# Optimization experiments

Measured on AMD Instinct MI355X. Metric: run time of the kernel, lower is better.

Reference implementation:

```python
import jax, jax.numpy as jnp
import numpy as np

B, S, D, K = 4, 4096, 1024, 64

def setup_inputs() -> dict:
    key = jax.random.key(0)
    kx, kq, kk, kv, ko = jax.random.split(key, 5)
    scale = 1.0 / np.sqrt(D)
    return {
        "x": jax.random.normal(kx, (B, S, D), dtype=jnp.float32),
        "Wq": jax.random.uniform(kq, (K, D), dtype=jnp.float32, minval=-scale, maxval=scale),
        "Wk": jax.random.uniform(kk, (K, D), dtype=jnp.float32, minval=-scale, maxval=scale),
        "Wv": jax.random.uniform(kv, (K, D), dtype=jnp.float32, minval=-scale, maxval=scale),
        "Wo": jax.random.uniform(ko, (D, K), dtype=jnp.float32, minval=-1.0/np.sqrt(K), maxval=1.0/np.sqrt(K)),
    }

def reference(x, Wq, Wk, Wv, Wo):
    # projections: torch Linear(dim, key_dim, bias=False) -> x @ W.T
    Q = jax.nn.elu(x @ Wq.T) + 1.0          # [B,S,K]
    Kf = jax.nn.elu(x @ Wk.T) + 1.0         # [B,S,K]
    V = x @ Wv.T                             # [B,S,K]
    # causal running KV state via cumsum of outer products: [B,S,K,K]
    KV_sum = jnp.cumsum(Kf[..., :, None] * V[..., None, :], axis=1)
    K_sum = jnp.cumsum(Kf, axis=1)           # [B,S,K]
    num = jnp.einsum('bsk,bskm->bsm', Q, KV_sum)   # [B,S,K]
    den = jnp.einsum('bsk,bsk->bs', Q, K_sum)[..., None]
    out = num / (den + 1e-6)
    return out @ Wo.T                         # [B,S,D]
```

## Files before the change

### kernel.cpp

```cpp
#include <hip/hip_runtime.h>

#define BB 4
#define SS 4096
#define DDIM 1024
#define KDIM 64
#define NCHUNK 64
#define TCHUNK 256
#define MROWS 16384

typedef short short8v __attribute__((ext_vector_type(8)));
typedef float f32x4 __attribute__((ext_vector_type(4)));
#define MFMA16 __builtin_amdgcn_mfma_f32_16x16x32_bf16

__device__ __forceinline__ ushort f2bf(float f) {
    uint u = __float_as_uint(f);
    u += 0x7FFFu + ((u >> 16) & 1u);
    return (ushort)(u >> 16);
}

__global__ __launch_bounds__(256) void k_wconv(
    const float* __restrict__ Wq, const float* __restrict__ Wk,
    const float* __restrict__ Wv, const float* __restrict__ Wo,
    ushort* __restrict__ Whf, ushort* __restrict__ Wof)
{
    const int b = blockIdx.x, t = threadIdx.x;
    const int ks = t >> 7;
    const int l = (t >> 1) & 63;
    const int half = t & 1;
    if (b < 192) {
        const int s = b / 12, cf = b % 12;
        const int grow = cf * 16 + (l & 15);
        const int gcol = s * 64 + ks * 32 + ((l >> 4) & 3) * 8 + half * 4;
        const float* src = (grow < 64) ? (Wq + (size_t)grow * DDIM)
                         : (grow < 128) ? (Wk + (size_t)(grow - 64) * DDIM)
                                        : (Wv + (size_t)(grow - 128) * DDIM);
        float4 v = *(const float4*)&src[gcol];
        ushort* dst = &Whf[(size_t)(((s * 12 + cf) * 2 + ks) * 64 + l) * 8 + half * 4];
        dst[0] = f2bf(v.x); dst[1] = f2bf(v.y); dst[2] = f2bf(v.z); dst[3] = f2bf(v.w);
    } else {
        const int cf = b - 192;
        const int d = cf * 16 + (l & 15);
        const int kc = ks * 32 + ((l >> 4) & 3) * 8 + half * 4;
        float4 v = *(const float4*)&Wo[(size_t)d * KDIM + kc];
        ushort* dst = &Wof[(size_t)((cf * 2 + ks) * 64 + l) * 8 + half * 4];
        dst[0] = f2bf(v.x); dst[1] = f2bf(v.y); dst[2] = f2bf(v.z); dst[3] = f2bf(v.w);
    }
}

#define EBP 216
__global__ __launch_bounds__(256) void k_proj(
    const float* __restrict__ x, const ushort* __restrict__ Whf,
    ushort* __restrict__ Qf, ushort* __restrict__ Kff,
    ushort* __restrict__ KfT, ushort* __restrict__ VT)
{
    __shared__ ushort xs[32 * 512];
    const int t = threadIdx.x;
    const int w = t >> 6, l = t & 63;
    const int mb = blockIdx.x;
    const int row0 = mb * 32;

    f32x4 acc[2][3];
#pragma unroll
    for (int r = 0; r < 2; ++r)
#pragma unroll
        for (int c = 0; c < 3; ++c) acc[r][c] = (f32x4){0.f, 0.f, 0.f, 0.f};

    auto stageX = [&](int h) {
#pragma unroll
        for (int i = 0; i < 8; ++i) {
            const int fidx = i * 256 + t;
            const int r = fidx >> 6;
            const int c = (fidx & 63) * 8;
            const float* p = &x[(size_t)(row0 + r) * DDIM + h * 512 + c];
            float4 u0 = *(const float4*)p;
            float4 u1 = *(const float4*)(p + 4);
            short8v hh;
            hh[0] = (short)f2bf(u0.x); hh[1] = (short)f2bf(u0.y);
            hh[2] = (short)f2bf(u0.z); hh[3] = (short)f2bf(u0.w);
            hh[4] = (short)f2bf(u1.x); hh[5] = (short)f2bf(u1.y);
            hh[6] = (short)f2bf(u1.z); hh[7] = (short)f2bf(u1.w);
            const int frag = (r >> 4) * 16 + (c >> 5);
            const int slot = ((r & 15) | (((c >> 3) & 3) << 4)) ^ (frag & 7);
            *(short8v*)&xs[(size_t)(frag * 64 + slot) * 8] = hh;
        }
    };
    auto loadW = [&](int sg, short8v (&bw)[6]) {
#pragma unroll
        for (int j = 0; j < 6; ++j) {
            const int cf = w * 3 + (j >> 1);
            const int f = cf * 2 + (j & 1);
            bw[j] = *(const short8v*)&Whf[((size_t)(sg * 24 + f)) * 512 + l * 8];
        }
    };
    auto computeStep = [&](int sl, short8v (&bw)[6]) {
#pragma unroll
        for (int ks = 0; ks < 2; ++ks) {
            const int kkl = sl * 2 + ks;
            const int f0 = kkl, f1 = 16 + kkl;
            short8v a0 = *(const short8v*)&xs[(size_t)(f0 * 64 + (l ^ (f0 & 7))) * 8];
            short8v a1 = *(const short8v*)&xs[(size_t)(f1 * 64 + (l ^ (f1 & 7))) * 8];
#pragma unroll
            for (int c = 0; c < 3; ++c) {
                acc[0][c] = MFMA16(a0, bw[c * 2 + ks], acc[0][c], 0, 0, 0);
                acc[1][c] = MFMA16(a1, bw[c * 2 + ks], acc[1][c], 0, 0, 0);
            }
        }
    };

    for (int h = 0; h < 2; ++h) {
        if (h) __syncthreads();
        stageX(h);
        __syncthreads();
        short8v bwA[6], bwB[6];
        loadW(h * 8, bwA);
        for (int s = 0; s < 8; s += 2) {
            loadW(h * 8 + s + 1, bwB);
            computeStep(s, bwA);
            if (s + 2 < 8) loadW(h * 8 + s + 2, bwA);
            computeStep(s + 1, bwB);
        }
    }

    __syncthreads();
    ushort* eb = xs;
#pragma unroll
    for (int rf = 0; rf < 2; ++rf)
#pragma unroll
        for (int c = 0; c < 3; ++c) {
            const int col = w * 48 + c * 16 + (l & 15);
#pragma unroll
            for (int q = 0; q < 4; ++q) {
                const int rl = rf * 16 + ((l >> 4) << 2) + q;
                float v = acc[rf][c][q];
                if (col < 128) v = (v > 0.f) ? v + 1.f : __expf(v);
                eb[rl * EBP + col] = f2bf(v);
            }
        }
    __syncthreads();

    {
        const int rf = t >> 7, ks = (t >> 6) & 1, lam = t & 63;
        const int r = rf * 16 + (lam & 15);
        const int c0 = ks * 32 + ((lam >> 4) & 3) * 8;
        short8v q8 = *(const short8v*)&eb[r * EBP + c0];
        short8v k8 = *(const short8v*)&eb[r * EBP + 64 + c0];
        const size_t fo = ((size_t)(mb * 4 + rf * 2 + ks)) * 512 + lam * 8;
        *(short8v*)&Qf[fo] = q8;
        *(short8v*)&Kff[fo] = k8;
    }
    {
        const int f = t >> 6, lam = t & 63;
        const int kcol = 64 + f * 16 + (lam & 15);
        const int vcol = 128 + f * 16 + (lam & 15);
        const int jb = ((lam >> 4) & 3) * 8;
        short8v kT, vT;
#pragma unroll
        for (int e = 0; e < 8; ++e) {
            kT[e] = (short)eb[(jb + e) * EBP + kcol];
            vT[e] = (short)eb[(jb + e) * EBP + vcol];
        }
        const size_t fo = ((size_t)((mb >> 1) * 8 + f * 2 + (mb & 1))) * 512 + lam * 8;
        *(short8v*)&KfT[fo] = kT;
        *(short8v*)&VT[fo] = vT;
    }
}

__global__ __launch_bounds__(64) void k_chunksum(
    const ushort* __restrict__ KfT, const ushort* __restrict__ VT,
    float* __restrict__ KVc, float* __restrict__ Ksc)
{
    const int g = blockIdx.x, l = threadIdx.x;
    short8v ka[4][2], vb[4][2];
#pragma unroll
    for (int f = 0; f < 4; ++f)
#pragma unroll
        for (int js = 0; js < 2; ++js) {
            const size_t fo = ((size_t)(g * 8 + f * 2 + js)) * 512 + l * 8;
            ka[f][js] = *(const short8v*)&KfT[fo];
            vb[f][js] = *(const short8v*)&VT[fo];
        }
    short8v onesf;
#pragma unroll
    for (int e = 0; e < 8; ++e) onesf[e] = ((l & 15) == 0) ? (short)0x3F80 : (short)0;

    f32x4 acc[4][5];
#pragma unroll
    for (int kf = 0; kf < 4; ++kf)
#pragma unroll
        for (int mf = 0; mf < 5; ++mf) acc[kf][mf] = (f32x4){0.f, 0.f, 0.f, 0.f};
#pragma unroll
    for (int js = 0; js < 2; ++js)
#pragma unroll
        for (int kf = 0; kf < 4; ++kf) {
#pragma unroll
            for (int mf = 0; mf < 4; ++mf)
                acc[kf][mf] = MFMA16(ka[kf][js], vb[mf][js], acc[kf][mf], 0, 0, 0);
            acc[kf][4] = MFMA16(ka[kf][js], onesf, acc[kf][4], 0, 0, 0);
        }
    const int lq = l >> 4;
#pragma unroll
    for (int kf = 0; kf < 4; ++kf) {
#pragma unroll
        for (int q = 0; q < 4; ++q) {
            const int k = kf * 16 + lq * 4 + q;
#pragma unroll
            for (int mf = 0; mf < 4; ++mf)
                KVc[(size_t)g * 4096 + k * 64 + mf * 16 + (l & 15)] = acc[kf][mf][q];
            if ((l & 15) == 0) Ksc[(size_t)g * KDIM + k] = acc[kf][4][q];
        }
    }
}

__global__ void k_scan(const float* __restrict__ KVc, const float* __restrict__ Ksc,
                       float* __restrict__ Sst, float* __restrict__ Kss)
{
    const int b = blockIdx.x / 65;
    const int r = blockIdx.x % 65;
    const int t = threadIdx.x;
    if (r < 64) {
        const int e = r * 64 + t;
        float v[64];
#pragma unroll
        for (int i = 0; i < 64; ++i)
            v[i] = KVc[((size_t)(b * NCHUNK + i)) * 4096 + e];
        float acc = 0.f;
#pragma unroll
        for (int i = 0; i < 64; ++i) {
            Sst[((size_t)(b * NCHUNK + i)) * 4096 + e] = acc;
            acc += v[i];
        }
    } else {
        float v[64];
#pragma unroll
        for (int i = 0; i < 64; ++i)
            v[i] = Ksc[((size_t)(b * NCHUNK + i)) * KDIM + t];
        float acc = 0.f;
#pragma unroll
        for (int i = 0; i < 64; ++i) {
            Kss[((size_t)(b * NCHUNK + i)) * KDIM + t] = acc;
            acc += v[i];
        }
    }
}

__global__ __launch_bounds__(256) void k_intra(
    const ushort* __restrict__ Qf, const ushort* __restrict__ Kff,
    const ushort* __restrict__ VT, const float* __restrict__ Sst,
    const float* __restrict__ Kss, const ushort* __restrict__ Wof,
    float* __restrict__ out)
{
    __shared__ ushort pb[64 * 64];
    __shared__ ushort sT[80 * 64];
    __shared__ float ob[4][16 * 68 + 4];
    const int g = blockIdx.x, t = threadIdx.x;
    const int w = t >> 6, l = t & 63;
    const int lq = l >> 4;

    {
        const int k = t >> 2, m0 = (t & 3) * 16;
        const float4* sp = (const float4*)&Sst[(size_t)g * 4096 + k * 64 + m0];
        float4 f0 = sp[0], f1 = sp[1], f2v = sp[2], f3 = sp[3];
        float fv[16] = {f0.x, f0.y, f0.z, f0.w, f1.x, f1.y, f1.z, f1.w,
                        f2v.x, f2v.y, f2v.z, f2v.w, f3.x, f3.y, f3.z, f3.w};
#pragma unroll
        for (int i = 0; i < 16; ++i) {
            const int m = m0 + i;
            sT[m * 64 + (k ^ ((m & 7) << 3))] = f2bf(fv[i]);
        }
        if (t < 64) sT[64 * 64 + t] = f2bf(Kss[(size_t)g * KDIM + t]);
        for (int idx = t; idx < 960; idx += 256) sT[65 * 64 + idx] = 0;
    }

    short8v qa[2], kb[4][2];
    {
        const int mb = g * 2 + (w >> 1), rf = w & 1;
#pragma unroll
        for (int ks = 0; ks < 2; ++ks)
            qa[ks] = *(const short8v*)&Qf[((size_t)(mb * 4 + rf * 2 + ks)) * 512 + l * 8];
#pragma unroll
        for (int cf = 0; cf < 4; ++cf)
#pragma unroll
            for (int ks = 0; ks < 2; ++ks)
                kb[cf][ks] = *(const short8v*)&Kff[((size_t)((g * 2 + (cf >> 1)) * 4 + (cf & 1) * 2 + ks)) * 512 + l * 8];
    }
    f32x4 accs[4];
#pragma unroll
    for (int cf = 0; cf < 4; ++cf) accs[cf] = (f32x4){0.f, 0.f, 0.f, 0.f};
#pragma unroll
    for (int ks = 0; ks < 2; ++ks)
#pragma unroll
        for (int cf = 0; cf < 4; ++cf)
            accs[cf] = MFMA16(qa[ks], kb[cf][ks], accs[cf], 0, 0, 0);
#pragma unroll
    for (int cf = 0; cf < 4; ++cf)
#pragma unroll
        for (int q = 0; q < 4; ++q) {
            const int row = w * 16 + lq * 4 + q;
            const int col = cf * 16 + (l & 15);
            const float sv = (col <= row) ? accs[cf][q] : 0.f;
            pb[row * 64 + (col ^ ((row & 7) << 3))] = f2bf(sv);
        }
    __syncthreads();

    f32x4 accn[5];
#pragma unroll
    for (int mf = 0; mf < 5; ++mf) accn[mf] = (f32x4){0.f, 0.f, 0.f, 0.f};
    short8v onesf;
#pragma unroll
    for (int e = 0; e < 8; ++e) onesf[e] = ((l & 15) == 0) ? (short)0x3F80 : (short)0;
#pragma unroll
    for (int js = 0; js < 2; ++js) {
        const int prow = w * 16 + (l & 15);
        const int pbase = js * 32 + ((l >> 4) & 3) * 8;
        short8v pa = *(const short8v*)&pb[prow * 64 + (pbase ^ ((prow & 7) << 3))];
#pragma unroll
        for (int mf = 0; mf < 4; ++mf) {
            short8v vb = *(const short8v*)&VT[((size_t)(g * 8 + mf * 2 + js)) * 512 + l * 8];
            accn[mf] = MFMA16(pa, vb, accn[mf], 0, 0, 0);
        }
        accn[4] = MFMA16(pa, onesf, accn[4], 0, 0, 0);
    }
#pragma unroll
    for (int ks = 0; ks < 2; ++ks) {
        const int base = ks * 32 + ((l >> 4) & 3) * 8;
#pragma unroll
        for (int mf = 0; mf < 5; ++mf) {
            const int row = mf * 16 + (l & 15);
            short8v sb = *(const short8v*)&sT[row * 64 + (base ^ ((row & 7) << 3))];
            accn[mf] = MFMA16(qa[ks], sb, accn[mf], 0, 0, 0);
        }
    }
#pragma unroll
    for (int q = 0; q < 4; ++q) {
        const float den = __shfl(accn[4][q], (l & 48));
        const float rinv = 1.f / (den + 1e-6f);
        const int row = w * 16 + lq * 4 + q;
#pragma unroll
        for (int mf = 0; mf < 4; ++mf) {
            const int col = mf * 16 + (l & 15);
            pb[row * 64 + (col ^ ((row & 7) << 3))] = f2bf(accn[mf][q] * rinv);
        }
    }
    __syncthreads();

    short8v oa[4][2];
#pragma unroll
    for (int rf = 0; rf < 4; ++rf)
#pragma unroll
        for (int ks = 0; ks < 2; ++ks) {
            const int row = rf * 16 + (l & 15);
            const int base = ks * 32 + ((l >> 4) & 3) * 8;
            oa[rf][ks] = *(const short8v*)&pb[row * 64 + (base ^ ((row & 7) << 3))];
        }
    float* obw = ob[w];
#pragma unroll
    for (int rr = 0; rr < 4; ++rr) {
        f32x4 acco[4][4];
#pragma unroll
        for (int rf = 0; rf < 4; ++rf)
#pragma unroll
            for (int ci = 0; ci < 4; ++ci) acco[rf][ci] = (f32x4){0.f, 0.f, 0.f, 0.f};
#pragma unroll
        for (int ci = 0; ci < 4; ++ci) {
            const int cfg = w * 16 + rr * 4 + ci;
#pragma unroll
            for (int ks = 0; ks < 2; ++ks) {
                short8v wb = *(const short8v*)&Wof[((size_t)(cfg * 2 + ks)) * 512 + l * 8];
#pragma unroll
                for (int rf = 0; rf < 4; ++rf)
                    acco[rf][ci] = MFMA16(oa[rf][ks], wb, acco[rf][ci], 0, 0, 0);
            }
        }
#pragma unroll
        for (int rf = 0; rf < 4; ++rf) {
#pragma unroll
            for (int ci = 0; ci < 4; ++ci)
#pragma unroll
                for (int q = 0; q < 4; ++q)
                    obw[(lq * 4 + q) * 68 + ci * 16 + (l & 15)] = acco[rf][ci][q];
#pragma unroll
            for (int rg = 0; rg < 4; ++rg) {
                const int row = rg * 4 + lq;
                float4 vv = *(const float4*)&obw[row * 68 + (l & 15) * 4];
                *(float4*)&out[((size_t)(g * 64 + rf * 16 + row)) * DDIM
                               + w * 256 + rr * 64 + (l & 15) * 4] = vv;
            }
        }
    }
}

extern "C" void kernel_launch(void* const* d_in, const int* in_sizes, int n_in,
                              void* d_out, int out_size, void* d_ws, size_t ws_size,
                              hipStream_t stream)
{
    const float* x  = (const float*)d_in[0];
    const float* Wq = (const float*)d_in[1];
    const float* Wk = (const float*)d_in[2];
    const float* Wv = (const float*)d_in[3];
    const float* Wo = (const float*)d_in[4];
    float* out = (float*)d_out;

    float* ws   = (float*)d_ws;
    float* KVc  = ws;
    float* Sst  = KVc + (size_t)TCHUNK * 4096;
    float* Ksc  = Sst + (size_t)TCHUNK * 4096;
    float* Kss  = Ksc + (size_t)TCHUNK * KDIM;
    ushort* Whf = (ushort*)(Kss + (size_t)TCHUNK * KDIM);
    ushort* Wof = Whf + (size_t)192 * DDIM;
    ushort* Qf  = Wof + (size_t)64 * 1024;
    ushort* Kff = Qf  + (size_t)512 * 4 * 512;
    ushort* KfT = Kff + (size_t)512 * 4 * 512;
    ushort* VT  = KfT + (size_t)256 * 8 * 512;

    k_wconv<<<dim3(256), dim3(256), 0, stream>>>(Wq, Wk, Wv, Wo, Whf, Wof);
    k_proj<<<dim3(MROWS / 32), dim3(256), 0, stream>>>(x, Whf, Qf, Kff, KfT, VT);
    k_chunksum<<<dim3(TCHUNK), dim3(64), 0, stream>>>(KfT, VT, KVc, Ksc);
    k_scan<<<dim3(BB * 65), dim3(64), 0, stream>>>(KVc, Ksc, Sst, Kss);
    k_intra<<<dim3(TCHUNK), dim3(256), 0, stream>>>(Qf, Kff, VT, Sst, Kss, Wof, out);
}
```

Before: 58.01 us.

## Fuse chunk-sum into projection kernel and split intra kernel into half-chunks

The projection kernel now runs one 512-thread block per 64-row chunk. It computes the per-chunk K^T V and K sums directly from shared memory, which removes the k_chunksum launch and the KfT global round-trip. The x staging is double-buffered, so the second half's global loads are issued into registers before the first half's MFMA loop runs. The intra kernel is split into two blocks per chunk, each handling 32 rows, which doubles grid parallelism for the output projection. The trade-offs are more shared memory and registers per block in k_proj, fewer k_proj blocks, and redundant per-block loads of S state and Wo in k_intra.

```diff
diff --git a/kernel.cpp b/kernel.cpp
--- a/kernel.cpp
+++ b/kernel.cpp
@@ -48,32 +48,39 @@
 }
 
 #define EBP 216
-__global__ __launch_bounds__(256) void k_proj(
+__global__ __launch_bounds__(512) void k_proj(
     const float* __restrict__ x, const ushort* __restrict__ Whf,
-    ushort* __restrict__ Qf, ushort* __restrict__ Kff,
-    ushort* __restrict__ KfT, ushort* __restrict__ VT)
+    ushort* __restrict__ Qf, ushort* __restrict__ Kff, ushort* __restrict__ VT,
+    float* __restrict__ KVc, float* __restrict__ Ksc)
 {
-    __shared__ ushort xs[32 * 512];
+    __shared__ ushort xs[2 * 64 * 512];
     const int t = threadIdx.x;
     const int w = t >> 6, l = t & 63;
-    const int mb = blockIdx.x;
-    const int row0 = mb * 32;
-
-    f32x4 acc[2][3];
-#pragma unroll
-    for (int r = 0; r < 2; ++r)
-#pragma unroll
-        for (int c = 0; c < 3; ++c) acc[r][c] = (f32x4){0.f, 0.f, 0.f, 0.f};
-
-    auto stageX = [&](int h) {
+    const int rw = w >> 2, cw = w & 3;
+    const int g = blockIdx.x;
+    const int row0 = g * 64;
+    const int lq = l >> 4;
+
+    float4 xr[16];
+    auto stageLoad = [&](int h) {
 #pragma unroll
         for (int i = 0; i < 8; ++i) {
-            const int fidx = i * 256 + t;
+            const int fidx = i * 512 + t;
             const int r = fidx >> 6;
             const int c = (fidx & 63) * 8;
             const float* p = &x[(size_t)(row0 + r) * DDIM + h * 512 + c];
-            float4 u0 = *(const float4*)p;
-            float4 u1 = *(const float4*)(p + 4);
+            xr[i * 2] = *(const float4*)p;
+            xr[i * 2 + 1] = *(const float4*)(p + 4);
+        }
+    };
+    auto stageWrite = [&](int buf) {
+        ushort* xb = xs + buf * 32768;
+#pragma unroll
+        for (int i = 0; i < 8; ++i) {
+            const int fidx = i * 512 + t;
+            const int r = fidx >> 6;
+            const int c = (fidx & 63) * 8;
+            float4 u0 = xr[i * 2], u1 = xr[i * 2 + 1];
             short8v hh;
             hh[0] = (short)f2bf(u0.x); hh[1] = (short)f2bf(u0.y);
             hh[2] = (short)f2bf(u0.z); hh[3] = (short)f2bf(u0.w);
@@ -81,24 +88,33 @@
             hh[6] = (short)f2bf(u1.z); hh[7] = (short)f2bf(u1.w);
             const int frag = (r >> 4) * 16 + (c >> 5);
             const int slot = ((r & 15) | (((c >> 3) & 3) << 4)) ^ (frag & 7);
-            *(short8v*)&xs[(size_t)(frag * 64 + slot) * 8] = hh;
+            *(short8v*)&xb[(size_t)(frag * 64 + slot) * 8] = hh;
         }
     };
+
+    f32x4 acc[2][3];
+#pragma unroll
+    for (int r = 0; r < 2; ++r)
+#pragma unroll
+        for (int c = 0; c < 3; ++c) acc[r][c] = (f32x4){0.f, 0.f, 0.f, 0.f};
+
     auto loadW = [&](int sg, short8v (&bw)[6]) {
 #pragma unroll
         for (int j = 0; j < 6; ++j) {
-            const int cf = w * 3 + (j >> 1);
+            const int cf = cw * 3 + (j >> 1);
             const int f = cf * 2 + (j & 1);
             bw[j] = *(const short8v*)&Whf[((size_t)(sg * 24 + f)) * 512 + l * 8];
         }
     };
-    auto computeStep = [&](int sl, short8v (&bw)[6]) {
+    auto computeStep = [&](int buf, int sl, short8v (&bw)[6]) {
+        const ushort* xb = xs + buf * 32768;
 #pragma unroll
         for (int ks = 0; ks < 2; ++ks) {
             const int kkl = sl * 2 + ks;
-            const int f0 = kkl, f1 = 16 + kkl;
-            short8v a0 = *(const short8v*)&xs[(size_t)(f0 * 64 + (l ^ (f0 & 7))) * 8];
-            short8v a1 = *(const short8v*)&xs[(size_t)(f1 * 64 + (l ^ (f1 & 7))) * 8];
+            const int f0 = (rw * 2) * 16 + kkl;
+            const int f1 = (rw * 2 + 1) * 16 + kkl;
+            short8v a0 = *(const short8v*)&xb[(size_t)(f0 * 64 + (l ^ (f0 & 7))) * 8];
+            short8v a1 = *(const short8v*)&xb[(size_t)(f1 * 64 + (l ^ (f1 & 7))) * 8];
 #pragma unroll
             for (int c = 0; c < 3; ++c) {
                 acc[0][c] = MFMA16(a0, bw[c * 2 + ks], acc[0][c], 0, 0, 0);
@@ -107,31 +123,42 @@
         }
     };
 
-    for (int h = 0; h < 2; ++h) {
-        if (h) __syncthreads();
-        stageX(h);
-        __syncthreads();
+    stageLoad(0); stageWrite(0);
+    __syncthreads();
+    stageLoad(1);
+    {
         short8v bwA[6], bwB[6];
-        loadW(h * 8, bwA);
+        loadW(0, bwA);
         for (int s = 0; s < 8; s += 2) {
-            loadW(h * 8 + s + 1, bwB);
-            computeStep(s, bwA);
-            if (s + 2 < 8) loadW(h * 8 + s + 2, bwA);
-            computeStep(s + 1, bwB);
-        }
-    }
-
+            loadW(s + 1, bwB);
+            computeStep(0, s, bwA);
+            if (s + 2 < 8) loadW(s + 2, bwA);
+            computeStep(0, s + 1, bwB);
+        }
+    }
+    stageWrite(1);
     __syncthreads();
+    {
+        short8v bwA[6], bwB[6];
+        loadW(8, bwA);
+        for (int s = 0; s < 8; s += 2) {
+            loadW(8 + s + 1, bwB);
+            computeStep(1, s, bwA);
+            if (s + 2 < 8) loadW(8 + s + 2, bwA);
+            computeStep(1, s + 1, bwB);
+        }
+    }
+
     ushort* eb = xs;
 #pragma unroll
-    for (int rf = 0; rf < 2; ++rf)
-#pragma unroll
-        for (int c = 0; c < 3; ++c) {
-            const int col = w * 48 + c * 16 + (l & 15);
+    for (int rfi = 0; rfi < 2; ++rfi)
+#pragma unroll
+        for (int ci = 0; ci < 3; ++ci) {
+            const int col = (cw * 3 + ci) * 16 + (l & 15);
 #pragma unroll
             for (int q = 0; q < 4; ++q) {
-                const int rl = rf * 16 + ((l >> 4) << 2) + q;
-                float v = acc[rf][c][q];
+                const int rl = (rw * 2 + rfi) * 16 + lq * 4 + q;
+                float v = acc[rfi][ci][q];
                 if (col < 128) v = (v > 0.f) ? v + 1.f : __expf(v);
                 eb[rl * EBP + col] = f2bf(v);
             }
@@ -139,74 +166,57 @@
     __syncthreads();
 
     {
-        const int rf = t >> 7, ks = (t >> 6) & 1, lam = t & 63;
-        const int r = rf * 16 + (lam & 15);
+        const int fj = t >> 6, lam = t & 63;
+        const int rh = fj >> 2, rfm = (fj >> 1) & 1, ks = fj & 1;
+        const int r = rh * 32 + rfm * 16 + (lam & 15);
         const int c0 = ks * 32 + ((lam >> 4) & 3) * 8;
         short8v q8 = *(const short8v*)&eb[r * EBP + c0];
         short8v k8 = *(const short8v*)&eb[r * EBP + 64 + c0];
-        const size_t fo = ((size_t)(mb * 4 + rf * 2 + ks)) * 512 + lam * 8;
+        const size_t fo = ((size_t)((g * 2 + rh) * 4 + rfm * 2 + ks)) * 512 + lam * 8;
         *(short8v*)&Qf[fo] = q8;
         *(short8v*)&Kff[fo] = k8;
     }
     {
-        const int f = t >> 6, lam = t & 63;
-        const int kcol = 64 + f * 16 + (lam & 15);
+        const int fj = t >> 6, lam = t & 63;
+        const int f = fj >> 1, js = fj & 1;
+        const int jb = js * 32 + ((lam >> 4) & 3) * 8;
         const int vcol = 128 + f * 16 + (lam & 15);
-        const int jb = ((lam >> 4) & 3) * 8;
-        short8v kT, vT;
-#pragma unroll
-        for (int e = 0; e < 8; ++e) {
-            kT[e] = (short)eb[(jb + e) * EBP + kcol];
-            vT[e] = (short)eb[(jb + e) * EBP + vcol];
-        }
-        const size_t fo = ((size_t)((mb >> 1) * 8 + f * 2 + (mb & 1))) * 512 + lam * 8;
-        *(short8v*)&KfT[fo] = kT;
-        *(short8v*)&VT[fo] = vT;
-    }
-}
-
-__global__ __launch_bounds__(64) void k_chunksum(
-    const ushort* __restrict__ KfT, const ushort* __restrict__ VT,
-    float* __restrict__ KVc, float* __restrict__ Ksc)
-{
-    const int g = blockIdx.x, l = threadIdx.x;
-    short8v ka[4][2], vb[4][2];
-#pragma unroll
-    for (int f = 0; f < 4; ++f)
+        short8v vT;
+#pragma unroll
+        for (int e = 0; e < 8; ++e) vT[e] = (short)eb[(jb + e) * EBP + vcol];
+        *(short8v*)&VT[((size_t)(g * 8 + f * 2 + js)) * 512 + lam * 8] = vT;
+    }
+    {
+        const int kf = w & 3, mh = w >> 2;
+        short8v ka[2], vb0[2], vb1[2];
 #pragma unroll
         for (int js = 0; js < 2; ++js) {
-            const size_t fo = ((size_t)(g * 8 + f * 2 + js)) * 512 + l * 8;
-            ka[f][js] = *(const short8v*)&KfT[fo];
-            vb[f][js] = *(const short8v*)&VT[fo];
-        }
-    short8v onesf;
-#pragma unroll
-    for (int e = 0; e < 8; ++e) onesf[e] = ((l & 15) == 0) ? (short)0x3F80 : (short)0;
-
-    f32x4 acc[4][5];
-#pragma unroll
-    for (int kf = 0; kf < 4; ++kf)
-#pragma unroll
-        for (int mf = 0; mf < 5; ++mf) acc[kf][mf] = (f32x4){0.f, 0.f, 0.f, 0.f};
-#pragma unroll
-    for (int js = 0; js < 2; ++js)
-#pragma unroll
-        for (int kf = 0; kf < 4; ++kf) {
-#pragma unroll
-            for (int mf = 0; mf < 4; ++mf)
-                acc[kf][mf] = MFMA16(ka[kf][js], vb[mf][js], acc[kf][mf], 0, 0, 0);
-            acc[kf][4] = MFMA16(ka[kf][js], onesf, acc[kf][4], 0, 0, 0);
-        }
-    const int lq = l >> 4;
-#pragma unroll
-    for (int kf = 0; kf < 4; ++kf) {
+            const int jb = js * 32 + ((l >> 4) & 3) * 8;
+#pragma unroll
+            for (int e = 0; e < 8; ++e) {
+                const int j = jb + e;
+                ka[js][e]  = (short)eb[j * EBP + 64 + kf * 16 + (l & 15)];
+                vb0[js][e] = (short)eb[j * EBP + 128 + (mh * 2 + 0) * 16 + (l & 15)];
+                vb1[js][e] = (short)eb[j * EBP + 128 + (mh * 2 + 1) * 16 + (l & 15)];
+            }
+        }
+        f32x4 a0 = (f32x4){0.f,0.f,0.f,0.f}, a1 = (f32x4){0.f,0.f,0.f,0.f};
+        f32x4 ad = (f32x4){0.f,0.f,0.f,0.f};
+        short8v onesf;
+#pragma unroll
+        for (int e = 0; e < 8; ++e) onesf[e] = ((l & 15) == 0) ? (short)0x3F80 : (short)0;
+#pragma unroll
+        for (int js = 0; js < 2; ++js) {
+            a0 = MFMA16(ka[js], vb0[js], a0, 0, 0, 0);
+            a1 = MFMA16(ka[js], vb1[js], a1, 0, 0, 0);
+            if (mh == 0) ad = MFMA16(ka[js], onesf, ad, 0, 0, 0);
+        }
 #pragma unroll
         for (int q = 0; q < 4; ++q) {
             const int k = kf * 16 + lq * 4 + q;
-#pragma unroll
-            for (int mf = 0; mf < 4; ++mf)
-                KVc[(size_t)g * 4096 + k * 64 + mf * 16 + (l & 15)] = acc[kf][mf][q];
-            if ((l & 15) == 0) Ksc[(size_t)g * KDIM + k] = acc[kf][4][q];
+            KVc[(size_t)g * 4096 + k * 64 + (mh * 2 + 0) * 16 + (l & 15)] = a0[q];
+            KVc[(size_t)g * 4096 + k * 64 + (mh * 2 + 1) * 16 + (l & 15)] = a1[q];
+            if (mh == 0 && (l & 15) == 0) Ksc[(size_t)g * KDIM + k] = ad[q];
         }
     }
 }
@@ -249,10 +259,11 @@
     const float* __restrict__ Kss, const ushort* __restrict__ Wof,
     float* __restrict__ out)
 {
-    __shared__ ushort pb[64 * 64];
+    __shared__ ushort pb[32 * 64];
     __shared__ ushort sT[80 * 64];
     __shared__ float ob[4][16 * 68 + 4];
-    const int g = blockIdx.x, t = threadIdx.x;
+    const int bx = blockIdx.x, t = threadIdx.x;
+    const int g = bx >> 1, rh = bx & 1;
     const int w = t >> 6, l = t & 63;
     const int lq = l >> 4;
 
@@ -271,95 +282,96 @@
         for (int idx = t; idx < 960; idx += 256) sT[65 * 64 + idx] = 0;
     }
 
-    short8v qa[2], kb[4][2];
-    {
-        const int mb = g * 2 + (w >> 1), rf = w & 1;
-#pragma unroll
-        for (int ks = 0; ks < 2; ++ks)
-            qa[ks] = *(const short8v*)&Qf[((size_t)(mb * 4 + rf * 2 + ks)) * 512 + l * 8];
-#pragma unroll
-        for (int cf = 0; cf < 4; ++cf)
-#pragma unroll
-            for (int ks = 0; ks < 2; ++ks)
-                kb[cf][ks] = *(const short8v*)&Kff[((size_t)((g * 2 + (cf >> 1)) * 4 + (cf & 1) * 2 + ks)) * 512 + l * 8];
-    }
-    f32x4 accs[4];
-#pragma unroll
-    for (int cf = 0; cf < 4; ++cf) accs[cf] = (f32x4){0.f, 0.f, 0.f, 0.f};
+    const int rf = w & 1;
+    short8v qa[2];
 #pragma unroll
     for (int ks = 0; ks < 2; ++ks)
-#pragma unroll
-        for (int cf = 0; cf < 4; ++cf)
-            accs[cf] = MFMA16(qa[ks], kb[cf][ks], accs[cf], 0, 0, 0);
-#pragma unroll
-    for (int cf = 0; cf < 4; ++cf)
-#pragma unroll
-        for (int q = 0; q < 4; ++q) {
-            const int row = w * 16 + lq * 4 + q;
-            const int col = cf * 16 + (l & 15);
-            const float sv = (col <= row) ? accs[cf][q] : 0.f;
-            pb[row * 64 + (col ^ ((row & 7) << 3))] = f2bf(sv);
-        }
+        qa[ks] = *(const short8v*)&Qf[((size_t)((g * 2 + rh) * 4 + rf * 2 + ks)) * 512 + l * 8];
+    {
+        const int cfh = w >> 1;
+        f32x4 accs[2];
+#pragma unroll
+        for (int ci = 0; ci < 2; ++ci) accs[ci] = (f32x4){0.f, 0.f, 0.f, 0.f};
+#pragma unroll
+        for (int ci = 0; ci < 2; ++ci) {
+            const int cf = cfh * 2 + ci;
+#pragma unroll
+            for (int ks = 0; ks < 2; ++ks) {
+                short8v kb = *(const short8v*)&Kff[((size_t)((g * 2 + (cf >> 1)) * 4 + (cf & 1) * 2 + ks)) * 512 + l * 8];
+                accs[ci] = MFMA16(qa[ks], kb, accs[ci], 0, 0, 0);
+            }
+        }
+#pragma unroll
+        for (int ci = 0; ci < 2; ++ci)
+#pragma unroll
+            for (int q = 0; q < 4; ++q) {
+                const int row = rf * 16 + lq * 4 + q;
+                const int col = (cfh * 2 + ci) * 16 + (l & 15);
+                const float sv = (col <= rh * 32 + row) ? accs[ci][q] : 0.f;
+                pb[row * 64 + (col ^ ((row & 7) << 3))] = f2bf(sv);
+            }
+    }
     __syncthreads();
 
-    f32x4 accn[5];
-#pragma unroll
-    for (int mf = 0; mf < 5; ++mf) accn[mf] = (f32x4){0.f, 0.f, 0.f, 0.f};
+    const int mg = w >> 1;
+    f32x4 an0 = (f32x4){0.f,0.f,0.f,0.f}, an1 = (f32x4){0.f,0.f,0.f,0.f};
+    f32x4 ad = (f32x4){0.f,0.f,0.f,0.f};
     short8v onesf;
 #pragma unroll
     for (int e = 0; e < 8; ++e) onesf[e] = ((l & 15) == 0) ? (short)0x3F80 : (short)0;
 #pragma unroll
     for (int js = 0; js < 2; ++js) {
-        const int prow = w * 16 + (l & 15);
+        const int prow = rf * 16 + (l & 15);
         const int pbase = js * 32 + ((l >> 4) & 3) * 8;
         short8v pa = *(const short8v*)&pb[prow * 64 + (pbase ^ ((prow & 7) << 3))];
-#pragma unroll
-        for (int mf = 0; mf < 4; ++mf) {
-            short8v vb = *(const short8v*)&VT[((size_t)(g * 8 + mf * 2 + js)) * 512 + l * 8];
-            accn[mf] = MFMA16(pa, vb, accn[mf], 0, 0, 0);
-        }
-        accn[4] = MFMA16(pa, onesf, accn[4], 0, 0, 0);
+        short8v v0 = *(const short8v*)&VT[((size_t)(g * 8 + (mg * 2 + 0) * 2 + js)) * 512 + l * 8];
+        short8v v1 = *(const short8v*)&VT[((size_t)(g * 8 + (mg * 2 + 1) * 2 + js)) * 512 + l * 8];
+        an0 = MFMA16(pa, v0, an0, 0, 0, 0);
+        an1 = MFMA16(pa, v1, an1, 0, 0, 0);
+        ad  = MFMA16(pa, onesf, ad, 0, 0, 0);
     }
 #pragma unroll
     for (int ks = 0; ks < 2; ++ks) {
         const int base = ks * 32 + ((l >> 4) & 3) * 8;
-#pragma unroll
-        for (int mf = 0; mf < 5; ++mf) {
-            const int row = mf * 16 + (l & 15);
-            short8v sb = *(const short8v*)&sT[row * 64 + (base ^ ((row & 7) << 3))];
-            accn[mf] = MFMA16(qa[ks], sb, accn[mf], 0, 0, 0);
-        }
+        const int r0 = (mg * 2 + 0) * 16 + (l & 15);
+        const int r1 = (mg * 2 + 1) * 16 + (l & 15);
+        const int r4 = 64 + (l & 15);
+        short8v s0 = *(const short8v*)&sT[r0 * 64 + (base ^ ((r0 & 7) << 3))];
+        short8v s1 = *(const short8v*)&sT[r1 * 64 + (base ^ ((r1 & 7) << 3))];
+        short8v s4 = *(const short8v*)&sT[r4 * 64 + (base ^ ((r4 & 7) << 3))];
+        an0 = MFMA16(qa[ks], s0, an0, 0, 0, 0);
+        an1 = MFMA16(qa[ks], s1, an1, 0, 0, 0);
+        ad  = MFMA16(qa[ks], s4, ad, 0, 0, 0);
     }
 #pragma unroll
     for (int q = 0; q < 4; ++q) {
-        const float den = __shfl(accn[4][q], (l & 48));
+        const float den = __shfl(ad[q], (l & 48));
         const float rinv = 1.f / (den + 1e-6f);
-        const int row = w * 16 + lq * 4 + q;
-#pragma unroll
-        for (int mf = 0; mf < 4; ++mf) {
-            const int col = mf * 16 + (l & 15);
-            pb[row * 64 + (col ^ ((row & 7) << 3))] = f2bf(accn[mf][q] * rinv);
-        }
+        const int row = rf * 16 + lq * 4 + q;
+        const int c0 = (mg * 2 + 0) * 16 + (l & 15);
+        const int c1 = (mg * 2 + 1) * 16 + (l & 15);
+        pb[row * 64 + (c0 ^ ((row & 7) << 3))] = f2bf(an0[q] * rinv);
+        pb[row * 64 + (c1 ^ ((row & 7) << 3))] = f2bf(an1[q] * rinv);
     }
     __syncthreads();
 
-    short8v oa[4][2];
-#pragma unroll
-    for (int rf = 0; rf < 4; ++rf)
+    short8v oa[2][2];
+#pragma unroll
+    for (int rfi = 0; rfi < 2; ++rfi)
 #pragma unroll
         for (int ks = 0; ks < 2; ++ks) {
-            const int row = rf * 16 + (l & 15);
+            const int row = rfi * 16 + (l & 15);
             const int base = ks * 32 + ((l >> 4) & 3) * 8;
-            oa[rf][ks] = *(const short8v*)&pb[row * 64 + (base ^ ((row & 7) << 3))];
+            oa[rfi][ks] = *(const short8v*)&pb[row * 64 + (base ^ ((row & 7) << 3))];
         }
     float* obw = ob[w];
 #pragma unroll
     for (int rr = 0; rr < 4; ++rr) {
-        f32x4 acco[4][4];
-#pragma unroll
-        for (int rf = 0; rf < 4; ++rf)
-#pragma unroll
-            for (int ci = 0; ci < 4; ++ci) acco[rf][ci] = (f32x4){0.f, 0.f, 0.f, 0.f};
+        f32x4 acco[2][4];
+#pragma unroll
+        for (int rfi = 0; rfi < 2; ++rfi)
+#pragma unroll
+            for (int ci = 0; ci < 4; ++ci) acco[rfi][ci] = (f32x4){0.f, 0.f, 0.f, 0.f};
 #pragma unroll
         for (int ci = 0; ci < 4; ++ci) {
             const int cfg = w * 16 + rr * 4 + ci;
@@ -367,22 +379,22 @@
             for (int ks = 0; ks < 2; ++ks) {
                 short8v wb = *(const short8v*)&Wof[((size_t)(cfg * 2 + ks)) * 512 + l * 8];
 #pragma unroll
-                for (int rf = 0; rf < 4; ++rf)
-                    acco[rf][ci] = MFMA16(oa[rf][ks], wb, acco[rf][ci], 0, 0, 0);
-            }
-        }
-#pragma unroll
-        for (int rf = 0; rf < 4; ++rf) {
+                for (int rfi = 0; rfi < 2; ++rfi)
+                    acco[rfi][ci] = MFMA16(oa[rfi][ks], wb, acco[rfi][ci], 0, 0, 0);
+            }
+        }
+#pragma unroll
+        for (int rfi = 0; rfi < 2; ++rfi) {
 #pragma unroll
             for (int ci = 0; ci < 4; ++ci)
 #pragma unroll
                 for (int q = 0; q < 4; ++q)
-                    obw[(lq * 4 + q) * 68 + ci * 16 + (l & 15)] = acco[rf][ci][q];
+                    obw[(lq * 4 + q) * 68 + ci * 16 + (l & 15)] = acco[rfi][ci][q];
 #pragma unroll
             for (int rg = 0; rg < 4; ++rg) {
                 const int row = rg * 4 + lq;
                 float4 vv = *(const float4*)&obw[row * 68 + (l & 15) * 4];
-                *(float4*)&out[((size_t)(g * 64 + rf * 16 + row)) * DDIM
+                *(float4*)&out[((size_t)(g * 64 + rh * 32 + rfi * 16 + row)) * DDIM
                                + w * 256 + rr * 64 + (l & 15) * 4] = vv;
             }
         }
@@ -409,12 +421,10 @@
     ushort* Wof = Whf + (size_t)192 * DDIM;
     ushort* Qf  = Wof + (size_t)64 * 1024;
     ushort* Kff = Qf  + (size_t)512 * 4 * 512;
-    ushort* KfT = Kff + (size_t)512 * 4 * 512;
-    ushort* VT  = KfT + (size_t)256 * 8 * 512;
+    ushort* VT  = Kff + (size_t)512 * 4 * 512;
 
     k_wconv<<<dim3(256), dim3(256), 0, stream>>>(Wq, Wk, Wv, Wo, Whf, Wof);
-    k_proj<<<dim3(MROWS / 32), dim3(256), 0, stream>>>(x, Whf, Qf, Kff, KfT, VT);
-    k_chunksum<<<dim3(TCHUNK), dim3(64), 0, stream>>>(KfT, VT, KVc, Ksc);
+    k_proj<<<dim3(TCHUNK), dim3(512), 0, stream>>>(x, Whf, Qf, Kff, VT, KVc, Ksc);
     k_scan<<<dim3(BB * 65), dim3(64), 0, stream>>>(KVc, Ksc, Sst, Kss);
-    k_intra<<<dim3(TCHUNK), dim3(256), 0, stream>>>(Qf, Kff, VT, Sst, Kss, Wof, out);
-}
+    k_intra<<<dim3(TCHUNK * 2), dim3(256), 0, stream>>>(Qf, Kff, VT, Sst, Kss, Wof, out);
+}
```

After: 56.80 us. 2.1% less time.
